# Performance work log

Hardware: AMD Instinct MI355X
Metric: run time of the kernel (lower is better)

## Reference

```python
import jax, jax.numpy as jnp
import numpy as np

E = 100000   # num edges
N = 50000    # num nodes (eg_idx, v, t triples)
B = 64       # num queries / subgraphs
D = 128      # n_dims_in
ID = 4 * D   # concat of 4 embeddings
OD = 2 * D   # G output dims
K = 1000     # max_edges per eg_idx


def setup_inputs() -> dict:
    key = jax.random.key(0)
    ks = jax.random.split(key, 12)
    eg_idx = jnp.sort(jax.random.randint(ks[0], (E,), 0, B)).astype(jnp.int32)
    node_i = jax.random.randint(ks[1], (E,), 0, N).astype(jnp.int32)
    node_j = jax.random.randint(ks[2], (E,), 0, N).astype(jnp.int32)
    node_score = jax.random.uniform(ks[3], (N,), dtype=jnp.float32)
    memorized_embedding = jax.random.normal(ks[4], (N, D), dtype=jnp.float32)
    rel_emb = jax.random.normal(ks[5], (E, D), dtype=jnp.float32)
    query_src_ts_emb = jax.random.normal(ks[6], (B, D), dtype=jnp.float32)
    query_rel_emb = jax.random.normal(ks[7], (B, D), dtype=jnp.float32)
    # G params: left/right dense init ~ N(0, sqrt(2/in)), center xavier-ish
    Wl = jax.random.normal(ks[8], (ID, OD), dtype=jnp.float32) * np.sqrt(2.0 / ID)
    Wr = jax.random.normal(ks[9], (ID, OD), dtype=jnp.float32) * np.sqrt(2.0 / ID)
    Wc = jax.random.normal(ks[10], (OD, OD), dtype=jnp.float32) * np.sqrt(2.0 / (OD + OD))
    bl = jnp.zeros((OD,), jnp.float32)
    br = jnp.zeros((OD,), jnp.float32)
    bc = jnp.zeros((OD,), jnp.float32)
    return dict(eg_idx=eg_idx, node_i=node_i, node_j=node_j, node_score=node_score,
                memorized_embedding=memorized_embedding, rel_emb=rel_emb,
                query_src_ts_emb=query_src_ts_emb, query_rel_emb=query_rel_emb,
                Wl=Wl, bl=bl, Wr=Wr, br=br, Wc=Wc, bc=bc, k=K)


def _segment_softmax(logits, seg, num_segments):
    m = jax.ops.segment_max(logits, seg, num_segments=num_segments)
    e = jnp.exp(logits - m[seg])
    s = jax.ops.segment_sum(e, seg, num_segments=num_segments)
    return e / s[seg]


def _topk_keep_mask(scores, group, num_groups, k):
    # keep edge iff its score ranks < k within its group (per-eg_idx topk)
    n = scores.shape[0]
    order = jnp.lexsort((-scores, group))          # sort by group asc, score desc
    sorted_group = group[order]
    counts = jax.ops.segment_sum(jnp.ones((n,), jnp.int32), group, num_segments=num_groups)
    starts = jnp.cumsum(counts) - counts           # exclusive cumsum: group start offsets
    rank_in_group = jnp.arange(n) - starts[sorted_group]
    keep_sorted = rank_in_group < k
    return jnp.zeros((n,), bool).at[order].set(keep_sorted)


def reference(eg_idx, node_i, node_j, node_score, memorized_embedding, rel_emb,
              query_src_ts_emb, query_rel_emb, Wl, bl, Wr, br, Wc, bc, k):
    num_nodes = memorized_embedding.shape[0]
    num_groups = query_src_ts_emb.shape[0]
    # gather per-edge embeddings
    hvi = memorized_embedding[node_i]              # [E, D]
    hvj = memorized_embedding[node_j]
    q_src = query_src_ts_emb[eg_idx]               # [E, D]
    q_rel = query_rel_emb[eg_idx]
    # G: bilinear MLP attention
    left_x = jnp.concatenate([hvi, rel_emb, q_src, q_rel], axis=-1)   # [E, 4D]
    right_x = jnp.concatenate([hvj, rel_emb, q_src, q_rel], axis=-1)
    l = jax.nn.leaky_relu(left_x @ Wl + bl)                           # [E, 2D]
    r = jax.nn.leaky_relu(right_x @ Wr + br) @ Wc + bc
    transition_logits = jnp.sum(l * r, axis=-1)                       # [E]
    # segment softmax over source node (eg_idx, vi, ti)
    soft = _segment_softmax(transition_logits, node_i, num_nodes)
    src_att = node_score[node_i]
    target_att = soft * src_att
    # per-eg_idx top-k pruning (keep mask instead of ragged slicing)
    keep = _topk_keep_mask(target_att, eg_idx, num_groups, k).astype(target_att.dtype)
    # sum aggregation: scatter soft * target_att into target nodes over kept edges
    updated_node_score = jax.ops.segment_sum(keep * soft * target_att, node_j,
                                             num_segments=num_nodes)
    return updated_node_score
```

## Files before the change

kernel.cpp:

```cpp
#include <hip/hip_runtime.h>

#define DD   128
#define ODIM 256
#define TE   32
#define TSLICE 16

__device__ __forceinline__ float leaky(float v) { return v > 0.f ? v : 0.01f * v; }

__global__ void k_query(const float* __restrict__ qs, const float* __restrict__ qr,
                        const float* __restrict__ Wl, const float* __restrict__ bl,
                        const float* __restrict__ Wr, const float* __restrict__ br,
                        float* __restrict__ Ql, float* __restrict__ Qr)
{
    const int g = blockIdx.x, t = threadIdx.x;
    float al = bl[t], ar = br[t];
    const float* qsg = qs + (size_t)g * DD;
    const float* qrg = qr + (size_t)g * DD;
    for (int k = 0; k < DD; ++k) {
        float a = qsg[k], b = qrg[k];
        al = fmaf(a, Wl[(size_t)(256 + k) * ODIM + t], al);
        al = fmaf(b, Wl[(size_t)(384 + k) * ODIM + t], al);
        ar = fmaf(a, Wr[(size_t)(256 + k) * ODIM + t], ar);
        ar = fmaf(b, Wr[(size_t)(384 + k) * ODIM + t], ar);
    }
    Ql[(size_t)g * ODIM + t] = al;
    Qr[(size_t)g * ODIM + t] = ar;
}

#define FMA4(dst, xc, wv, j)                                \
    dst[j][0] = fmaf(xc, wv.x, dst[j][0]);                  \
    dst[j][1] = fmaf(xc, wv.y, dst[j][1]);                  \
    dst[j][2] = fmaf(xc, wv.z, dst[j][2]);                  \
    dst[j][3] = fmaf(xc, wv.w, dst[j][3]);

__global__ __launch_bounds__(256, 4)
void k_edge_logits(const int* __restrict__ eg_idx, const int* __restrict__ node_i,
                   const int* __restrict__ node_j,
                   const float* __restrict__ me, const float* __restrict__ rel,
                   const float* __restrict__ Wl, const float* __restrict__ Wr,
                   const float* __restrict__ Wc, const float* __restrict__ bc,
                   const float* __restrict__ Ql, const float* __restrict__ Qr,
                   float* __restrict__ logits, int E)
{
    __shared__ float s_a[TE][DD];
    __shared__ float s_b[TE][DD];
    __shared__ int   s_ni[TE], s_nj[TE], s_g[TE];

    const int tx = threadIdx.x;
    const int cg = tx & 63;
    const int er = tx >> 6;
    const int c0 = cg << 2;
    const int e0 = blockIdx.x * TE;
    const int eb = er * 8;

    if (tx < TE) {
        int e = e0 + tx;
        s_ni[tx] = (e < E) ? node_i[e] : -1;
        s_nj[tx] = (e < E) ? node_j[e] : -1;
        s_g[tx]  = (e < E) ? eg_idx[e] : 0;
    }
    __syncthreads();

    for (int it = tx; it < TE * DD / 4; it += 256) {
        int i  = it >> 5;
        int kk = (it & 31) << 2;
        float4 v = make_float4(0.f, 0.f, 0.f, 0.f);
        float4 h = v;
        if (e0 + i < E) {
            v = *(const float4*)(rel + (size_t)(e0 + i) * DD + kk);
            h = *(const float4*)(me + (size_t)s_nj[i] * DD + kk);
        }
        *(float4*)(&s_a[i][kk]) = v;
        *(float4*)(&s_b[i][kk]) = h;
    }
    __syncthreads();

    float acc[8][4];
#pragma unroll
    for (int j = 0; j < 8; ++j) { acc[j][0] = acc[j][1] = acc[j][2] = acc[j][3] = 0.f; }

    for (int k = 0; k < DD; k += 4) {
        const float* wp = Wr + (size_t)k * ODIM + c0;
        float4 w0 = *(const float4*)(wp);
        float4 w1 = *(const float4*)(wp + ODIM);
        float4 w2 = *(const float4*)(wp + 2 * ODIM);
        float4 w3 = *(const float4*)(wp + 3 * ODIM);
#pragma unroll
        for (int j = 0; j < 8; ++j) {
            float4 x = *(const float4*)(&s_b[eb + j][k]);
            FMA4(acc, x.x, w0, j) FMA4(acc, x.y, w1, j) FMA4(acc, x.z, w2, j) FMA4(acc, x.w, w3, j)
        }
    }
    for (int k = 0; k < DD; k += 4) {
        const float* wp = Wr + (size_t)(DD + k) * ODIM + c0;
        float4 w0 = *(const float4*)(wp);
        float4 w1 = *(const float4*)(wp + ODIM);
        float4 w2 = *(const float4*)(wp + 2 * ODIM);
        float4 w3 = *(const float4*)(wp + 3 * ODIM);
#pragma unroll
        for (int j = 0; j < 8; ++j) {
            float4 x = *(const float4*)(&s_a[eb + j][k]);
            FMA4(acc, x.x, w0, j) FMA4(acc, x.y, w1, j) FMA4(acc, x.z, w2, j) FMA4(acc, x.w, w3, j)
        }
    }

#pragma unroll
    for (int j = 0; j < 8; ++j) {
        int g = s_g[eb + j];
        float4 q = *(const float4*)(Qr + (size_t)g * ODIM + c0);
        acc[j][0] = leaky(acc[j][0] + q.x);
        acc[j][1] = leaky(acc[j][1] + q.y);
        acc[j][2] = leaky(acc[j][2] + q.z);
        acc[j][3] = leaky(acc[j][3] + q.w);
    }

    float uacc[8][4];
#pragma unroll
    for (int j = 0; j < 8; ++j) { uacc[j][0] = uacc[j][1] = uacc[j][2] = uacc[j][3] = 0.f; }

    __syncthreads();
    if (c0 < DD) {
#pragma unroll
        for (int j = 0; j < 8; ++j)
            *(float4*)(&s_b[eb + j][c0]) = make_float4(acc[j][0], acc[j][1], acc[j][2], acc[j][3]);
    }
    __syncthreads();
    for (int k = 0; k < DD; k += 4) {
        const float* wp = Wc + (size_t)k * ODIM + c0;
        float4 w0 = *(const float4*)(wp);
        float4 w1 = *(const float4*)(wp + ODIM);
        float4 w2 = *(const float4*)(wp + 2 * ODIM);
        float4 w3 = *(const float4*)(wp + 3 * ODIM);
#pragma unroll
        for (int j = 0; j < 8; ++j) {
            float4 x = *(const float4*)(&s_b[eb + j][k]);
            FMA4(uacc, x.x, w0, j) FMA4(uacc, x.y, w1, j) FMA4(uacc, x.z, w2, j) FMA4(uacc, x.w, w3, j)
        }
    }
    __syncthreads();
    if (c0 >= DD) {
#pragma unroll
        for (int j = 0; j < 8; ++j)
            *(float4*)(&s_b[eb + j][c0 - DD]) = make_float4(acc[j][0], acc[j][1], acc[j][2], acc[j][3]);
    }
    __syncthreads();
    for (int k = 0; k < DD; k += 4) {
        const float* wp = Wc + (size_t)(DD + k) * ODIM + c0;
        float4 w0 = *(const float4*)(wp);
        float4 w1 = *(const float4*)(wp + ODIM);
        float4 w2 = *(const float4*)(wp + 2 * ODIM);
        float4 w3 = *(const float4*)(wp + 3 * ODIM);
#pragma unroll
        for (int j = 0; j < 8; ++j) {
            float4 x = *(const float4*)(&s_b[eb + j][k]);
            FMA4(uacc, x.x, w0, j) FMA4(uacc, x.y, w1, j) FMA4(uacc, x.z, w2, j) FMA4(uacc, x.w, w3, j)
        }
    }

    {
        float4 bcv = *(const float4*)(bc + c0);
#pragma unroll
        for (int j = 0; j < 8; ++j) {
            uacc[j][0] += bcv.x; uacc[j][1] += bcv.y;
            uacc[j][2] += bcv.z; uacc[j][3] += bcv.w;
        }
    }

    __syncthreads();
    for (int it = tx; it < TE * DD / 4; it += 256) {
        int i  = it >> 5;
        int kk = (it & 31) << 2;
        float4 h = make_float4(0.f, 0.f, 0.f, 0.f);
        if (e0 + i < E) h = *(const float4*)(me + (size_t)s_ni[i] * DD + kk);
        *(float4*)(&s_b[i][kk]) = h;
    }
    __syncthreads();

#pragma unroll
    for (int j = 0; j < 8; ++j) { acc[j][0] = acc[j][1] = acc[j][2] = acc[j][3] = 0.f; }

    for (int k = 0; k < DD; k += 4) {
        const float* wp = Wl + (size_t)k * ODIM + c0;
        float4 w0 = *(const float4*)(wp);
        float4 w1 = *(const float4*)(wp + ODIM);
        float4 w2 = *(const float4*)(wp + 2 * ODIM);
        float4 w3 = *(const float4*)(wp + 3 * ODIM);
#pragma unroll
        for (int j = 0; j < 8; ++j) {
            float4 x = *(const float4*)(&s_b[eb + j][k]);
            FMA4(acc, x.x, w0, j) FMA4(acc, x.y, w1, j) FMA4(acc, x.z, w2, j) FMA4(acc, x.w, w3, j)
        }
    }
    for (int k = 0; k < DD; k += 4) {
        const float* wp = Wl + (size_t)(DD + k) * ODIM + c0;
        float4 w0 = *(const float4*)(wp);
        float4 w1 = *(const float4*)(wp + ODIM);
        float4 w2 = *(const float4*)(wp + 2 * ODIM);
        float4 w3 = *(const float4*)(wp + 3 * ODIM);
#pragma unroll
        for (int j = 0; j < 8; ++j) {
            float4 x = *(const float4*)(&s_a[eb + j][k]);
            FMA4(acc, x.x, w0, j) FMA4(acc, x.y, w1, j) FMA4(acc, x.z, w2, j) FMA4(acc, x.w, w3, j)
        }
    }

#pragma unroll
    for (int j = 0; j < 8; ++j) {
        int g = s_g[eb + j];
        float4 q = *(const float4*)(Ql + (size_t)g * ODIM + c0);
        float p = leaky(acc[j][0] + q.x) * uacc[j][0]
                + leaky(acc[j][1] + q.y) * uacc[j][1]
                + leaky(acc[j][2] + q.z) * uacc[j][2]
                + leaky(acc[j][3] + q.w) * uacc[j][3];
#pragma unroll
        for (int off = 32; off > 0; off >>= 1) p += __shfl_down(p, off);
        if (cg == 0) {
            int e = e0 + eb + j;
            if (e < E) logits[e] = p;
        }
    }
}

__device__ __forceinline__ unsigned f32_enc(float f) {
    unsigned u = __float_as_uint(f);
    return (u & 0x80000000u) ? ~u : (u | 0x80000000u);
}
__device__ __forceinline__ float f32_dec(unsigned x) {
    return (x & 0x80000000u) ? __uint_as_float(x & 0x7fffffffu) : __uint_as_float(~x);
}

__global__ void k_segmax(const float* __restrict__ logits, const int* __restrict__ ni,
                         unsigned* __restrict__ segmax, int E)
{
    int e = blockIdx.x * 256 + threadIdx.x;
    if (e >= E) return;
    atomicMax(&segmax[ni[e]], f32_enc(logits[e]));
}

__global__ void k_expsum(const float* __restrict__ logits, const int* __restrict__ ni,
                         const unsigned* __restrict__ segmax,
                         float* __restrict__ eexp, float* __restrict__ segsum, int E)
{
    int e = blockIdx.x * 256 + threadIdx.x;
    if (e >= E) return;
    float m = f32_dec(segmax[ni[e]]);
    float v = expf(logits[e] - m);
    eexp[e] = v;
    atomicAdd(&segsum[ni[e]], v);
}

__global__ void k_soft(const float* __restrict__ eexp, const float* __restrict__ segsum,
                       const int* __restrict__ ni, const float* __restrict__ node_score,
                       float* __restrict__ soft, float* __restrict__ ta, int E)
{
    int e = blockIdx.x * 256 + threadIdx.x;
    if (e >= E) return;
    int n = ni[e];
    float s = eexp[e] / segsum[n];
    soft[e] = s;
    ta[e]   = s * node_score[n];
}

__global__ void k_starts(const int* __restrict__ eg, int E, int B, int* __restrict__ starts)
{
    int g = blockIdx.x * blockDim.x + threadIdx.x;
    if (g > B) return;
    int lo = 0, hi = E;
    while (lo < hi) { int mid = (lo + hi) >> 1; if (eg[mid] < g) lo = mid + 1; else hi = mid; }
    starts[g] = lo;
}

__global__ __launch_bounds__(256)
void k_topk(const int* __restrict__ starts, const int* __restrict__ node_j,
            const float* __restrict__ soft, const float* __restrict__ ta,
            const int* __restrict__ kptr, float* __restrict__ out)
{
    __shared__ float s_val[2048];
    const int g  = blockIdx.x / TSLICE;
    const int sl = blockIdx.x % TSLICE;
    const int gs = starts[g], ge = starts[g + 1];
    const int cnt = ge - gs;
    if (cnt <= 0) return;
    const int per = (cnt + TSLICE - 1) / TSLICE;
    const int c0  = sl * per;
    const int c1  = min(cnt, c0 + per);
    if (c0 >= cnt) return;
    const int K  = kptr[0];
    const int tx = threadIdx.x;

    for (int base = c0; base < c1; base += 256) {
        int   li  = base + tx;
        bool  act = li < c1;
        float mv  = act ? ta[gs + li] : 0.f;
        int   rank = 0;
        for (int t0 = 0; t0 < cnt; t0 += 2048) {
            int tlen = min(2048, cnt - t0);
            __syncthreads();
            for (int i = tx; i < tlen; i += 256) s_val[i] = ta[gs + t0 + i];
            __syncthreads();
            for (int i = 0; i < tlen; ++i) {
                float v  = s_val[i];
                int   gi = t0 + i;
                rank += (int)((v > mv) || (v == mv && gi < li));
            }
        }
        if (act && rank < K) {
            int e = gs + li;
            atomicAdd(&out[node_j[e]], soft[e] * ta[e]);
        }
    }
}

extern "C" void kernel_launch(void* const* d_in, const int* in_sizes, int n_in,
                              void* d_out, int out_size, void* d_ws, size_t ws_size,
                              hipStream_t stream)
{
    const int*   eg_idx     = (const int*)d_in[0];
    const int*   node_i     = (const int*)d_in[1];
    const int*   node_j     = (const int*)d_in[2];
    const float* node_score = (const float*)d_in[3];
    const float* me         = (const float*)d_in[4];
    const float* rel        = (const float*)d_in[5];
    const float* qs         = (const float*)d_in[6];
    const float* qr         = (const float*)d_in[7];
    const float* Wl         = (const float*)d_in[8];
    const float* bl         = (const float*)d_in[9];
    const float* Wr         = (const float*)d_in[10];
    const float* br         = (const float*)d_in[11];
    const float* Wc         = (const float*)d_in[12];
    const float* bc         = (const float*)d_in[13];
    const int*   kptr       = (const int*)d_in[14];

    const int E = in_sizes[0];
    const int N = in_sizes[3];
    const int B = in_sizes[6] / DD;

    float* ws      = (float*)d_ws;
    float* logits  = ws;
    float* eexp    = ws + (size_t)E;
    float* soft    = ws + 2 * (size_t)E;
    float* ta      = ws + 3 * (size_t)E;
    unsigned* segmax = (unsigned*)(ws + 4 * (size_t)E);
    float* segsum  = ws + 4 * (size_t)E + (size_t)N;
    float* Ql      = ws + 4 * (size_t)E + 2 * (size_t)N;
    float* Qr      = Ql + (size_t)B * ODIM;
    int*   starts  = (int*)(Qr + (size_t)B * ODIM);

    hipMemsetAsync(d_out, 0, (size_t)N * sizeof(float), stream);
    hipMemsetAsync(segmax, 0, (size_t)2 * N * sizeof(float), stream);

    k_query<<<B, 256, 0, stream>>>(qs, qr, Wl, bl, Wr, br, Ql, Qr);
    k_edge_logits<<<(E + TE - 1) / TE, 256, 0, stream>>>(eg_idx, node_i, node_j, me, rel,
                                                         Wl, Wr, Wc, bc, Ql, Qr, logits, E);
    int gE = (E + 255) / 256;
    k_segmax<<<gE, 256, 0, stream>>>(logits, node_i, segmax, E);
    k_expsum<<<gE, 256, 0, stream>>>(logits, node_i, segmax, eexp, segsum, E);
    k_soft<<<gE, 256, 0, stream>>>(eexp, segsum, node_i, node_score, soft, ta, E);
    k_starts<<<1, 128, 0, stream>>>(eg_idx, E, B, starts);
    k_topk<<<B * TSLICE, 256, 0, stream>>>(starts, node_j, soft, ta, kptr, (float*)d_out);
}
```

Measured before the change: 633.0 us.

## Precompute per-node left/right projections and gather them in the edge kernel

Measured after the change: 572.4 us. -9.6%, faster.

```diff
diff --git a/kernel.cpp b/kernel.cpp
--- a/kernel.cpp
+++ b/kernel.cpp
@@ -33,7 +33,223 @@
     dst[j][2] = fmaf(xc, wv.z, dst[j][2]);                  \
     dst[j][3] = fmaf(xc, wv.w, dst[j][3]);
 
-__global__ __launch_bounds__(256, 4)
+__global__ __launch_bounds__(256, 2)
+void k_nodepre(const float* __restrict__ me, const float* __restrict__ Wl,
+               const float* __restrict__ Wr, float* __restrict__ Xl,
+               float* __restrict__ Xr, int N)
+{
+    __shared__ float s_me[TE][DD];
+
+    const int tx = threadIdx.x;
+    const int cg = tx & 63;
+    const int er = tx >> 6;
+    const int c0 = cg << 2;
+    const int n0 = blockIdx.x * TE;
+    const int eb = er * 8;
+
+    for (int it = tx; it < TE * DD / 4; it += 256) {
+        int i  = it >> 5;
+        int kk = (it & 31) << 2;
+        float4 h = make_float4(0.f, 0.f, 0.f, 0.f);
+        if (n0 + i < N) h = *(const float4*)(me + (size_t)(n0 + i) * DD + kk);
+        *(float4*)(&s_me[i][kk]) = h;
+    }
+    __syncthreads();
+
+    float acc[8][4];
+#pragma unroll
+    for (int j = 0; j < 8; ++j) { acc[j][0] = acc[j][1] = acc[j][2] = acc[j][3] = 0.f; }
+    for (int k = 0; k < DD; k += 4) {
+        const float* wp = Wl + (size_t)k * ODIM + c0;
+        float4 w0 = *(const float4*)(wp);
+        float4 w1 = *(const float4*)(wp + ODIM);
+        float4 w2 = *(const float4*)(wp + 2 * ODIM);
+        float4 w3 = *(const float4*)(wp + 3 * ODIM);
+#pragma unroll
+        for (int j = 0; j < 8; ++j) {
+            float4 x = *(const float4*)(&s_me[eb + j][k]);
+            FMA4(acc, x.x, w0, j) FMA4(acc, x.y, w1, j) FMA4(acc, x.z, w2, j) FMA4(acc, x.w, w3, j)
+        }
+    }
+#pragma unroll
+    for (int j = 0; j < 8; ++j) {
+        int n = n0 + eb + j;
+        if (n < N)
+            *(float4*)(Xl + (size_t)n * ODIM + c0) = make_float4(acc[j][0], acc[j][1], acc[j][2], acc[j][3]);
+    }
+
+#pragma unroll
+    for (int j = 0; j < 8; ++j) { acc[j][0] = acc[j][1] = acc[j][2] = acc[j][3] = 0.f; }
+    for (int k = 0; k < DD; k += 4) {
+        const float* wp = Wr + (size_t)k * ODIM + c0;
+        float4 w0 = *(const float4*)(wp);
+        float4 w1 = *(const float4*)(wp + ODIM);
+        float4 w2 = *(const float4*)(wp + 2 * ODIM);
+        float4 w3 = *(const float4*)(wp + 3 * ODIM);
+#pragma unroll
+        for (int j = 0; j < 8; ++j) {
+            float4 x = *(const float4*)(&s_me[eb + j][k]);
+            FMA4(acc, x.x, w0, j) FMA4(acc, x.y, w1, j) FMA4(acc, x.z, w2, j) FMA4(acc, x.w, w3, j)
+        }
+    }
+#pragma unroll
+    for (int j = 0; j < 8; ++j) {
+        int n = n0 + eb + j;
+        if (n < N)
+            *(float4*)(Xr + (size_t)n * ODIM + c0) = make_float4(acc[j][0], acc[j][1], acc[j][2], acc[j][3]);
+    }
+}
+
+__global__ __launch_bounds__(256, 2)
+void k_edge_logits_pre(const int* __restrict__ eg_idx, const int* __restrict__ node_i,
+                       const int* __restrict__ node_j, const float* __restrict__ rel,
+                       const float* __restrict__ Wl, const float* __restrict__ Wr,
+                       const float* __restrict__ Wc, const float* __restrict__ bc,
+                       const float* __restrict__ Ql, const float* __restrict__ Qr,
+                       const float* __restrict__ Xl, const float* __restrict__ Xr,
+                       float* __restrict__ logits, int E)
+{
+    __shared__ float s_a[TE][DD];
+    __shared__ float s_b[TE][DD];
+    __shared__ int   s_ni[TE], s_nj[TE], s_g[TE];
+
+    const int tx = threadIdx.x;
+    const int cg = tx & 63;
+    const int er = tx >> 6;
+    const int c0 = cg << 2;
+    const int e0 = blockIdx.x * TE;
+    const int eb = er * 8;
+
+    if (tx < TE) {
+        int e = e0 + tx;
+        s_ni[tx] = (e < E) ? node_i[e] : 0;
+        s_nj[tx] = (e < E) ? node_j[e] : 0;
+        s_g[tx]  = (e < E) ? eg_idx[e] : 0;
+    }
+    __syncthreads();
+
+    for (int it = tx; it < TE * DD / 4; it += 256) {
+        int i  = it >> 5;
+        int kk = (it & 31) << 2;
+        float4 v = make_float4(0.f, 0.f, 0.f, 0.f);
+        if (e0 + i < E) v = *(const float4*)(rel + (size_t)(e0 + i) * DD + kk);
+        *(float4*)(&s_a[i][kk]) = v;
+    }
+    __syncthreads();
+
+    float acc[8][4];
+#pragma unroll
+    for (int j = 0; j < 8; ++j) { acc[j][0] = acc[j][1] = acc[j][2] = acc[j][3] = 0.f; }
+
+    for (int k = 0; k < DD; k += 4) {
+        const float* wp = Wr + (size_t)(DD + k) * ODIM + c0;
+        float4 w0 = *(const float4*)(wp);
+        float4 w1 = *(const float4*)(wp + ODIM);
+        float4 w2 = *(const float4*)(wp + 2 * ODIM);
+        float4 w3 = *(const float4*)(wp + 3 * ODIM);
+#pragma unroll
+        for (int j = 0; j < 8; ++j) {
+            float4 x = *(const float4*)(&s_a[eb + j][k]);
+            FMA4(acc, x.x, w0, j) FMA4(acc, x.y, w1, j) FMA4(acc, x.z, w2, j) FMA4(acc, x.w, w3, j)
+        }
+    }
+
+#pragma unroll
+    for (int j = 0; j < 8; ++j) {
+        int idx = eb + j;
+        float4 xr = *(const float4*)(Xr + (size_t)s_nj[idx] * ODIM + c0);
+        float4 q  = *(const float4*)(Qr + (size_t)s_g[idx] * ODIM + c0);
+        acc[j][0] = leaky(acc[j][0] + xr.x + q.x);
+        acc[j][1] = leaky(acc[j][1] + xr.y + q.y);
+        acc[j][2] = leaky(acc[j][2] + xr.z + q.z);
+        acc[j][3] = leaky(acc[j][3] + xr.w + q.w);
+    }
+
+    float uacc[8][4];
+#pragma unroll
+    for (int j = 0; j < 8; ++j) { uacc[j][0] = uacc[j][1] = uacc[j][2] = uacc[j][3] = 0.f; }
+
+    if (c0 < DD) {
+#pragma unroll
+        for (int j = 0; j < 8; ++j)
+            *(float4*)(&s_b[eb + j][c0]) = make_float4(acc[j][0], acc[j][1], acc[j][2], acc[j][3]);
+    }
+    __syncthreads();
+    for (int k = 0; k < DD; k += 4) {
+        const float* wp = Wc + (size_t)k * ODIM + c0;
+        float4 w0 = *(const float4*)(wp);
+        float4 w1 = *(const float4*)(wp + ODIM);
+        float4 w2 = *(const float4*)(wp + 2 * ODIM);
+        float4 w3 = *(const float4*)(wp + 3 * ODIM);
+#pragma unroll
+        for (int j = 0; j < 8; ++j) {
+            float4 x = *(const float4*)(&s_b[eb + j][k]);
+            FMA4(uacc, x.x, w0, j) FMA4(uacc, x.y, w1, j) FMA4(uacc, x.z, w2, j) FMA4(uacc, x.w, w3, j)
+        }
+    }
+    __syncthreads();
+    if (c0 >= DD) {
+#pragma unroll
+        for (int j = 0; j < 8; ++j)
+            *(float4*)(&s_b[eb + j][c0 - DD]) = make_float4(acc[j][0], acc[j][1], acc[j][2], acc[j][3]);
+    }
+    __syncthreads();
+    for (int k = 0; k < DD; k += 4) {
+        const float* wp = Wc + (size_t)(DD + k) * ODIM + c0;
+        float4 w0 = *(const float4*)(wp);
+        float4 w1 = *(const float4*)(wp + ODIM);
+        float4 w2 = *(const float4*)(wp + 2 * ODIM);
+        float4 w3 = *(const float4*)(wp + 3 * ODIM);
+#pragma unroll
+        for (int j = 0; j < 8; ++j) {
+            float4 x = *(const float4*)(&s_b[eb + j][k]);
+            FMA4(uacc, x.x, w0, j) FMA4(uacc, x.y, w1, j) FMA4(uacc, x.z, w2, j) FMA4(uacc, x.w, w3, j)
+        }
+    }
+
+    {
+        float4 bcv = *(const float4*)(bc + c0);
+#pragma unroll
+        for (int j = 0; j < 8; ++j) {
+            uacc[j][0] += bcv.x; uacc[j][1] += bcv.y;
+            uacc[j][2] += bcv.z; uacc[j][3] += bcv.w;
+        }
+    }
+
+#pragma unroll
+    for (int j = 0; j < 8; ++j) { acc[j][0] = acc[j][1] = acc[j][2] = acc[j][3] = 0.f; }
+    for (int k = 0; k < DD; k += 4) {
+        const float* wp = Wl + (size_t)(DD + k) * ODIM + c0;
+        float4 w0 = *(const float4*)(wp);
+        float4 w1 = *(const float4*)(wp + ODIM);
+        float4 w2 = *(const float4*)(wp + 2 * ODIM);
+        float4 w3 = *(const float4*)(wp + 3 * ODIM);
+#pragma unroll
+        for (int j = 0; j < 8; ++j) {
+            float4 x = *(const float4*)(&s_a[eb + j][k]);
+            FMA4(acc, x.x, w0, j) FMA4(acc, x.y, w1, j) FMA4(acc, x.z, w2, j) FMA4(acc, x.w, w3, j)
+        }
+    }
+
+#pragma unroll
+    for (int j = 0; j < 8; ++j) {
+        int idx = eb + j;
+        float4 xl = *(const float4*)(Xl + (size_t)s_ni[idx] * ODIM + c0);
+        float4 q  = *(const float4*)(Ql + (size_t)s_g[idx] * ODIM + c0);
+        float p = leaky(acc[j][0] + xl.x + q.x) * uacc[j][0]
+                + leaky(acc[j][1] + xl.y + q.y) * uacc[j][1]
+                + leaky(acc[j][2] + xl.z + q.z) * uacc[j][2]
+                + leaky(acc[j][3] + xl.w + q.w) * uacc[j][3];
+#pragma unroll
+        for (int off = 32; off > 0; off >>= 1) p += __shfl_down(p, off);
+        if (cg == 0) {
+            int e = e0 + eb + j;
+            if (e < E) logits[e] = p;
+        }
+    }
+}
+
+__global__ __launch_bounds__(256, 2)
 void k_edge_logits(const int* __restrict__ eg_idx, const int* __restrict__ node_i,
                    const int* __restrict__ node_j,
                    const float* __restrict__ me, const float* __restrict__ rel,
@@ -55,8 +271,8 @@
 
     if (tx < TE) {
         int e = e0 + tx;
-        s_ni[tx] = (e < E) ? node_i[e] : -1;
-        s_nj[tx] = (e < E) ? node_j[e] : -1;
+        s_ni[tx] = (e < E) ? node_i[e] : 0;
+        s_nj[tx] = (e < E) ? node_j[e] : 0;
         s_g[tx]  = (e < E) ? eg_idx[e] : 0;
     }
     __syncthreads();
@@ -345,13 +561,25 @@
     float* Ql      = ws + 4 * (size_t)E + 2 * (size_t)N;
     float* Qr      = Ql + (size_t)B * ODIM;
     int*   starts  = (int*)(Qr + (size_t)B * ODIM);
+    size_t base    = 4 * (size_t)E + 2 * (size_t)N + 2 * (size_t)B * ODIM + (size_t)(B + 1);
+    float* Xl      = ws + base;
+    float* Xr      = Xl + (size_t)N * ODIM;
+    size_t needed  = (base + 2 * (size_t)N * ODIM) * sizeof(float);
+    bool use_pre   = ws_size >= needed;
 
     hipMemsetAsync(d_out, 0, (size_t)N * sizeof(float), stream);
     hipMemsetAsync(segmax, 0, (size_t)2 * N * sizeof(float), stream);
 
     k_query<<<B, 256, 0, stream>>>(qs, qr, Wl, bl, Wr, br, Ql, Qr);
-    k_edge_logits<<<(E + TE - 1) / TE, 256, 0, stream>>>(eg_idx, node_i, node_j, me, rel,
-                                                         Wl, Wr, Wc, bc, Ql, Qr, logits, E);
+    if (use_pre) {
+        k_nodepre<<<(N + TE - 1) / TE, 256, 0, stream>>>(me, Wl, Wr, Xl, Xr, N);
+        k_edge_logits_pre<<<(E + TE - 1) / TE, 256, 0, stream>>>(eg_idx, node_i, node_j, rel,
+                                                                 Wl, Wr, Wc, bc, Ql, Qr,
+                                                                 Xl, Xr, logits, E);
+    } else {
+        k_edge_logits<<<(E + TE - 1) / TE, 256, 0, stream>>>(eg_idx, node_i, node_j, me, rel,
+                                                             Wl, Wr, Wc, bc, Ql, Qr, logits, E);
+    }
     int gE = (E + 255) / 256;
     k_segmax<<<gE, 256, 0, stream>>>(logits, node_i, segmax, E);
     k_expsum<<<gE, 256, 0, stream>>>(logits, node_i, segmax, eexp, segsum, E);
```
